# Kernel optimization log

Hardware: AMD Instinct MI355X
Metric: run time of the kernel (lower is better)

## Reference

```python
import jax, jax.numpy as jnp
import numpy as np

KERNEL_SIZES = (2, 3, 4, 5)
B, T = 128, 512
CH, EMB, CHID, HID = 128, 64, 128, 256


def conv1d_same(x, w, b):
    # x: [B, T, Cin], w: [K, Cin, Cout] -> [B, T, Cout]
    y = jax.lax.conv_general_dilated(
        x, w, window_strides=(1,), padding='SAME',
        dimension_numbers=('NWC', 'WIO', 'NWC'))
    return y + b


def gru_last_state(x, Wx, Wh, b_in, b_rec):
    # Keras GRU v2 (reset_after=True), gate order z, r, h. x: [B, T, C].
    H = Wh.shape[0]
    xw = jnp.einsum('btc,ch->bth', x, Wx) + b_in  # precompute input projections [B,T,3H]

    def step(h, xt):
        hw = h @ Wh + b_rec
        xz, xr, xh = jnp.split(xt, 3, axis=-1)
        hz, hr, hh = jnp.split(hw, 3, axis=-1)
        z = jax.nn.sigmoid(xz + hz)
        r = jax.nn.sigmoid(xr + hr)
        hc = jnp.tanh(xh + r * hh)
        return z * h + (1.0 - z) * hc, None

    h0 = jnp.zeros((x.shape[0], H), x.dtype)
    hT, _ = jax.lax.scan(step, h0, jnp.swapaxes(xw, 0, 1))  # scan over time
    return hT  # [B, H]


def setup_inputs() -> dict:
    key = jax.random.key(0)
    ks = jax.random.split(key, 16)
    inp = {}
    inp['X'] = jax.random.randint(ks[0], (B, T), 0, CH)
    inp['emb_table'] = jax.random.normal(ks[1], (CH, EMB), jnp.float32) * 0.05
    s_conv = 1.0 / np.sqrt(EMB)
    for i, k in enumerate(KERNEL_SIZES):
        inp[f'conv_w{k}'] = jax.random.normal(ks[2 + i], (k, EMB, CHID), jnp.float32) * s_conv
        inp[f'conv_b{k}'] = jnp.zeros((CHID,), jnp.float32)
    cin = CHID * len(KERNEL_SIZES)
    inp['gru_Wx'] = jax.random.normal(ks[10], (cin, 3 * HID), jnp.float32) * (1.0 / np.sqrt(cin))
    inp['gru_Wh'] = jax.random.normal(ks[11], (HID, 3 * HID), jnp.float32) * (1.0 / np.sqrt(HID))
    inp['gru_b_in'] = jnp.zeros((3 * HID,), jnp.float32)
    inp['gru_b_rec'] = jnp.zeros((3 * HID,), jnp.float32)
    return inp


def reference(X, emb_table, conv_w2, conv_b2, conv_w3, conv_b3, conv_w4, conv_b4,
              conv_w5, conv_b5, gru_Wx, gru_Wh, gru_b_in, gru_b_rec):
    xe = emb_table[X]  # [B, T, EMB]
    convs = [conv1d_same(xe, w, b) for (w, b) in
             ((conv_w2, conv_b2), (conv_w3, conv_b3), (conv_w4, conv_b4), (conv_w5, conv_b5))]
    xcat = jnp.concatenate(convs, axis=-1)  # [B, T, 4*CHID]
    return gru_last_state(xcat, gru_Wx, gru_Wh, gru_b_in, gru_b_rec)  # [B, HID]
```

## Files before the change

kernel.cpp:

```cpp
#include <hip/hip_runtime.h>
#include <hip/hip_bf16.h>


typedef float f32x4 __attribute__((ext_vector_type(4)));
typedef short s16x8 __attribute__((ext_vector_type(8)));
typedef int   i32x4 __attribute__((ext_vector_type(4)));
typedef unsigned short u16;
typedef unsigned int   u32;
typedef unsigned long long u64;

#define OFF_WC    0u
#define OFF_EMBW  983040u
#define OFF_BEFF  2949120u
#define OFF_WHP   2952192u
#define OFF_MODE  3345408u
#define OFF_HGP   3345472u
#define OFF_FLAG  3607616u
#define FS        516
#define WS_NEED   3624128u

__device__ __forceinline__ float bf2f(u16 v){
  unsigned u = ((unsigned)v) << 16; return __builtin_bit_cast(float, u);
}
__device__ __forceinline__ u16 f2bf(float f){
  unsigned u = __builtin_bit_cast(unsigned, f);
  unsigned r = u + 0x7FFFu + ((u >> 16) & 1u);
  return (u16)(r >> 16);
}
__device__ __forceinline__ float ldv(const void* p, int i, int m){
  return m ? ((const float*)p)[i] : bf2f(((const u16*)p)[i]);
}

__global__ void k_init(char* ws){
  int idx = blockIdx.x*256 + threadIdx.x;
  u32* hg = (u32*)(ws + OFF_HGP);
  if (idx < 65536) hg[idx] = 0u;
  int* fl = (int*)(ws + OFF_FLAG);
  if (idx < 8*FS) fl[idx] = ((idx % FS) == 0) ? 4 : 0;
}

__global__ void k_probe(const void* __restrict__ emb, char* ws){
  const u16* w = (const u16*)emb;
  const int ln = threadIdx.x;
  bool bad = false;
  for (int j = 0; j < 8; ++j){
    u16 v = w[ln*8 + j];
    if (((v >> 7) & 0xFF) >= 0x86) bad = true;
  }
  unsigned long long m = __ballot(bad);
  if (ln == 0) *(int*)(ws + OFF_MODE) = (__popcll(m) > 4) ? 1 : 0;
}

__global__ void k_wc(const void* __restrict__ w2, const void* __restrict__ w3,
                     const void* __restrict__ w4, const void* __restrict__ w5,
                     const void* __restrict__ Wx, char* ws){
  const int md = *(const int*)(ws + OFF_MODE);
  const int d = blockIdx.x >> 6;
  const int e = blockIdx.x & 63;
  const int j0 = threadIdx.x;
  const void* wv[4] = {w2,w3,w4,w5};
  const int Kk[4] = {2,3,4,5}, pd[4] = {0,1,1,2};
  float a0=0.f, a1=0.f, a2=0.f;
  for (int br=0; br<4; ++br){
    int k = d - 2 + pd[br];
    if (k < 0 || k >= Kk[br]) continue;
    const int wbase  = (k*64 + e)*128;
    const int wxbase = (br*128)*768;
    for (int c=0; c<128; ++c){
      float wcv = ldv(wv[br], wbase + c, md);
      a0 += wcv * ldv(Wx, wxbase + c*768 + j0      , md);
      a1 += wcv * ldv(Wx, wxbase + c*768 + j0 + 256, md);
      a2 += wcv * ldv(Wx, wxbase + c*768 + j0 + 512, md);
    }
  }
  float* o = (float*)(ws + OFF_WC) + (d*64 + e)*768;
  o[j0] = a0; o[j0+256] = a1; o[j0+512] = a2;
}

__global__ void k_beff(const void* __restrict__ b2, const void* __restrict__ b3,
                       const void* __restrict__ b4, const void* __restrict__ b5,
                       const void* __restrict__ Wx, const void* __restrict__ bin,
                       char* ws){
  const int md = *(const int*)(ws + OFF_MODE);
  int j = blockIdx.x*256 + threadIdx.x;
  if (j >= 768) return;
  const void* bv[4] = {b2,b3,b4,b5};
  float acc = ldv(bin, j, md);
  for (int br=0; br<4; ++br)
    for (int c=0; c<128; ++c)
      acc += ldv(bv[br], c, md) * ldv(Wx, (br*128 + c)*768 + j, md);
  ((float*)(ws + OFF_BEFF))[j] = acc;
}

__global__ void k_embw(const void* __restrict__ emb, char* ws){
  const int md = *(const int*)(ws + OFF_MODE);
  const int d = blockIdx.x >> 7, ch = blockIdx.x & 127;
  const float* wc = (const float*)(ws + OFF_WC) + d*64*768;
  float* ew = (float*)(ws + OFF_EMBW) + (size_t)(d*128 + ch)*768;
  const int j0 = threadIdx.x;
  float a0=0.f, a1=0.f, a2=0.f;
  for (int e=0; e<64; ++e){
    float ev = ldv(emb, ch*64 + e, md);
    a0 += ev*wc[e*768 + j0      ];
    a1 += ev*wc[e*768 + j0 + 256];
    a2 += ev*wc[e*768 + j0 + 512];
  }
  ew[j0] = a0; ew[j0+256] = a1; ew[j0+512] = a2;
}

__global__ void k_whp(const void* __restrict__ Wh, char* ws){
  const int md = *(const int*)(ws + OFF_MODE);
  const int j = blockIdx.x, k = threadIdx.x;
  ((u16*)(ws + OFF_WHP))[j*256 + k] = f2bf(ldv(Wh, k*768 + j, md));
}

__launch_bounds__(512, 1)
__global__ void k_gru(const int* __restrict__ X, const void* __restrict__ brec,
                      char* __restrict__ ws, void* __restrict__ outv){
  const int tid = threadIdx.x;
  const int w   = tid >> 6, ln = tid & 63;
  const int l15 = ln & 15, l4 = ln >> 4;
  const int g = blockIdx.x >> 2, r = blockIdx.x & 3;

  const int md = *(const int*)(ws + OFF_MODE);
  const float* embw = (const float*)(ws + OFF_EMBW);
  const float* beff = (const float*)(ws + OFF_BEFF);
  const u16*   whp  = (const u16*)(ws + OFF_WHP);
  u32* hgp = (u32*)(ws + OFF_HGP);
  int* flg = (int*)(ws + OFF_FLAG) + g*FS;

  __shared__ int   Xs[16*512];
  __shared__ float xwlds[2][16][196];
  __shared__ float hwp[2][16][196];
  __shared__ u16   hstage[2][16][272];

  for (int i = tid; i < 2048; i += 512)
    ((i32x4*)Xs)[i] = ((const i32x4*)(X + g*16*512))[i];

  const int qs = (w >> 2) * 4;
  s16x8 Bf[3][4];
  #pragma unroll
  for (int gg=0; gg<3; ++gg){
    const int col = gg*256 + r*64 + (w&3)*16 + l15;
    #pragma unroll
    for (int qi=0; qi<4; ++qi)
      Bf[gg][qi] = *(const s16x8*)(whp + col*256 + (qs+qi)*32 + l4*8);
  }

  const int c63 = tid & 63;
  const int tr  = (tid >> 6) & 7;
  const int hc  = r*64 + c63;
  const float br0 = ldv(brec,       hc, md);
  const float br1 = ldv(brec, 256 + hc, md);
  const float br2 = ldv(brec, 512 + hc, md);

  const int row1 = tid / 48,      rem1 = tid % 48;
  const int gg1  = rem1 / 16,     cc1  = rem1 % 16;
  const int cid2 = tid + 512;
  const int row2 = cid2 / 48,     rem2 = cid2 % 48;
  const int gg2  = rem2 / 16,     cc2  = rem2 % 16;
  const bool two = (tid < 256);
  const int gcol1 = gg1*256 + r*64 + cc1*4;
  const int gcol2 = gg2*256 + r*64 + cc2*4;
  const f32x4 be1 = *(const f32x4*)(beff + gcol1);
  const f32x4 be2 = *(const f32x4*)(beff + gcol2);

  const int srow = tid >> 5, sc0 = (tid & 31) * 8;

  __syncthreads();

  {
    f32x4 v1 = be1, v2 = be2;
    #pragma unroll
    for (int d=0; d<5; ++d){
      const int t = d - 2;
      if ((unsigned)t < 512u){
        const int ch1 = Xs[row1*512 + t] & 127;
        v1 += *(const f32x4*)(embw + (size_t)(d*128 + ch1)*768 + gcol1);
        if (two){
          const int ch2 = Xs[row2*512 + t] & 127;
          v2 += *(const f32x4*)(embw + (size_t)(d*128 + ch2)*768 + gcol2);
        }
      }
    }
    *(f32x4*)&xwlds[0][row1][gg1*64 + cc1*4] = v1;
    if (two) *(f32x4*)&xwlds[0][row2][gg2*64 + cc2*4] = v2;
  }
  float hpA = 0.f, hpB = 0.f;
  __syncthreads();

  for (int s = 0; s < 512; ++s){
    const int par = s & 1;

    {
      int guard = 0;
      while (__hip_atomic_load(&flg[s], __ATOMIC_RELAXED, __HIP_MEMORY_SCOPE_AGENT) < 4){
        if (++guard > (1<<23)) break;
      }
    }

    {
      const u32* hb = hgp + (unsigned)par*32768u + (unsigned)g*4096u
                      + (unsigned)srow*256u + (unsigned)sc0;
      u64 d0 = __hip_atomic_load((const u64*)hb+0, __ATOMIC_RELAXED, __HIP_MEMORY_SCOPE_AGENT);
      u64 d1 = __hip_atomic_load((const u64*)hb+1, __ATOMIC_RELAXED, __HIP_MEMORY_SCOPE_AGENT);
      u64 d2 = __hip_atomic_load((const u64*)hb+2, __ATOMIC_RELAXED, __HIP_MEMORY_SCOPE_AGENT);
      u64 d3 = __hip_atomic_load((const u64*)hb+3, __ATOMIC_RELAXED, __HIP_MEMORY_SCOPE_AGENT);
      u32 wd[8] = {(u32)d0,(u32)(d0>>32),(u32)d1,(u32)(d1>>32),
                   (u32)d2,(u32)(d2>>32),(u32)d3,(u32)(d3>>32)};
      s16x8 hi, lo;
      #pragma unroll
      for (int j=0; j<8; ++j){ hi[j] = (short)(wd[j] & 0xFFFFu); lo[j] = (short)(wd[j] >> 16); }
      *(s16x8*)&hstage[0][srow][sc0] = hi;
      *(s16x8*)&hstage[1][srow][sc0] = lo;
    }
    __syncthreads();

    f32x4 a0 = {0.f,0.f,0.f,0.f}, a1 = a0, a2 = a0;
    #pragma unroll
    for (int qi=0; qi<4; ++qi){
      const int kb = (qs+qi)*32 + l4*8;
      const s16x8 ahi = *(const s16x8*)&hstage[0][l15][kb];
      const s16x8 alo = *(const s16x8*)&hstage[1][l15][kb];
      a0 = __builtin_amdgcn_mfma_f32_16x16x32_bf16(ahi, Bf[0][qi], a0, 0,0,0);
      a1 = __builtin_amdgcn_mfma_f32_16x16x32_bf16(ahi, Bf[1][qi], a1, 0,0,0);
      a2 = __builtin_amdgcn_mfma_f32_16x16x32_bf16(ahi, Bf[2][qi], a2, 0,0,0);
      a0 = __builtin_amdgcn_mfma_f32_16x16x32_bf16(alo, Bf[0][qi], a0, 0,0,0);
      a1 = __builtin_amdgcn_mfma_f32_16x16x32_bf16(alo, Bf[1][qi], a1, 0,0,0);
      a2 = __builtin_amdgcn_mfma_f32_16x16x32_bf16(alo, Bf[2][qi], a2, 0,0,0);
    }
    {
      const int kh = w >> 2, sc = (w&3)*16 + l15;
      #pragma unroll
      for (int p=0; p<4; ++p){
        hwp[kh][l4*4+p][       sc] = a0[p];
        hwp[kh][l4*4+p][ 64 + sc] = a1[p];
        hwp[kh][l4*4+p][128 + sc] = a2[p];
      }
    }

    f32x4 n1, n2;
    if (s < 511){
      n1 = be1; n2 = be2;
      #pragma unroll
      for (int d=0; d<5; ++d){
        const int t = s - 1 + d;
        if ((unsigned)t < 512u){
          const int ch1 = Xs[row1*512 + t] & 127;
          n1 += *(const f32x4*)(embw + (size_t)(d*128 + ch1)*768 + gcol1);
          if (two){
            const int ch2 = Xs[row2*512 + t] & 127;
            n2 += *(const f32x4*)(embw + (size_t)(d*128 + ch2)*768 + gcol2);
          }
        }
      }
    }
    __syncthreads();

    float hnA, hnB;
    #pragma unroll
    for (int u=0; u<2; ++u){
      const int row = tr + u*8;
      const float hz = hwp[0][row][      c63] + hwp[1][row][      c63] + br0;
      const float hr = hwp[0][row][ 64 + c63] + hwp[1][row][ 64 + c63] + br1;
      const float hh = hwp[0][row][128 + c63] + hwp[1][row][128 + c63] + br2;
      const float xz = xwlds[par][row][      c63];
      const float xr = xwlds[par][row][ 64 + c63];
      const float xh = xwlds[par][row][128 + c63];
      const float hp = u ? hpB : hpA;
      const float z  = 1.f/(1.f + __expf(-(xz + hz)));
      const float rg = 1.f/(1.f + __expf(-(xr + hr)));
      const float pre = xh + rg*hh;
      const float e2  = __expf(-2.f*fabsf(pre));
      const float th  = __builtin_copysignf((1.f - e2)/(1.f + e2), pre);
      const float hn  = z*hp + (1.f - z)*th;
      if (u) hnB = hn; else hnA = hn;
    }
    hpA = hnA; hpB = hnB;

    if (s == 511){
      const int i0 = (g*16 + tr)*256 + hc;
      if (md){ ((float*)outv)[i0] = hnA; ((float*)outv)[i0 + 8*256] = hnB; }
      else   { ((u16*)outv)[i0] = f2bf(hnA); ((u16*)outv)[i0 + 8*256] = f2bf(hnB); }
    } else {
      u32* hb = hgp + (unsigned)(par^1)*32768u + (unsigned)g*4096u;
      #pragma unroll
      for (int u=0; u<2; ++u){
        const float hn = u ? hnB : hnA;
        const u32 bh = f2bf(hn);
        const u32 bl = f2bf(hn - bf2f((u16)bh));
        __hip_atomic_store(hb + (tr + u*8)*256 + hc, bh | (bl << 16),
                           __ATOMIC_RELAXED, __HIP_MEMORY_SCOPE_AGENT);
      }
      *(f32x4*)&xwlds[par^1][row1][gg1*64 + cc1*4] = n1;
      if (two) *(f32x4*)&xwlds[par^1][row2][gg2*64 + cc2*4] = n2;
    }

    __syncthreads();
    if (s < 511 && tid == 0)
      __hip_atomic_fetch_add(&flg[s+1], 1, __ATOMIC_RELEASE, __HIP_MEMORY_SCOPE_AGENT);
  }
}

extern "C" void kernel_launch(void* const* d_in, const int* in_sizes, int n_in,
                              void* d_out, int out_size, void* d_ws, size_t ws_size,
                              hipStream_t stream){
  const int* X = (const int*)d_in[0];
  char* ws = (char*)d_ws;
  if (ws_size < WS_NEED) return;

  k_init <<<288, 256, 0, stream>>>(ws);
  k_probe<<<  1,  64, 0, stream>>>(d_in[1], ws);
  k_wc   <<<320, 256, 0, stream>>>(d_in[2], d_in[4], d_in[6], d_in[8], d_in[10], ws);
  k_beff <<<  3, 256, 0, stream>>>(d_in[3], d_in[5], d_in[7], d_in[9], d_in[10], d_in[12], ws);
  k_embw <<<640, 256, 0, stream>>>(d_in[1], ws);
  k_whp  <<<768, 256, 0, stream>>>(d_in[11], ws);
  k_gru  <<< 32, 512, 0, stream>>>(X, d_in[13], ws, d_out);
}
```

Measured before the change: 2.350 ms.

## Replace per-step flag counters with sequence bits embedded in hidden-state words

Each hidden-state word now carries a parity sequence bit in the low bit of its bf16 residual half. Consumers spin directly on the data words until all sequence bits match the expected step parity. This removes the per-step global flag array, its release atomic, and the trailing block barrier, which shortens the cross-block handoff on the serial recurrence path. The cost is one mantissa bit lost in the low bf16 correction term, plus repeated polling of four 64-bit loads per thread instead of one flag load.

```diff
diff --git a/kernel.cpp b/kernel.cpp
--- a/kernel.cpp
+++ b/kernel.cpp
@@ -15,9 +15,7 @@
 #define OFF_WHP   2952192u
 #define OFF_MODE  3345408u
 #define OFF_HGP   3345472u
-#define OFF_FLAG  3607616u
-#define FS        516
-#define WS_NEED   3624128u
+#define WS_NEED   3607616u
 
 __device__ __forceinline__ float bf2f(u16 v){
   unsigned u = ((unsigned)v) << 16; return __builtin_bit_cast(float, u);
@@ -35,8 +33,6 @@
   int idx = blockIdx.x*256 + threadIdx.x;
   u32* hg = (u32*)(ws + OFF_HGP);
   if (idx < 65536) hg[idx] = 0u;
-  int* fl = (int*)(ws + OFF_FLAG);
-  if (idx < 8*FS) fl[idx] = ((idx % FS) == 0) ? 4 : 0;
 }
 
 __global__ void k_probe(const void* __restrict__ emb, char* ws){
@@ -127,7 +123,6 @@
   const float* beff = (const float*)(ws + OFF_BEFF);
   const u16*   whp  = (const u16*)(ws + OFF_WHP);
   u32* hgp = (u32*)(ws + OFF_HGP);
-  int* flg = (int*)(ws + OFF_FLAG) + g*FS;
 
   __shared__ int   Xs[16*512];
   __shared__ float xwlds[2][16][196];
@@ -192,25 +187,30 @@
   for (int s = 0; s < 512; ++s){
     const int par = s & 1;
 
+    const u32 em = (u32)((s >> 1) & 1);
+    const u32* hb = hgp + (unsigned)par*32768u + (unsigned)g*4096u
+                    + (unsigned)srow*256u + (unsigned)sc0;
+    u64 d0, d1, d2, d3;
     {
       int guard = 0;
-      while (__hip_atomic_load(&flg[s], __ATOMIC_RELAXED, __HIP_MEMORY_SCOPE_AGENT) < 4){
-        if (++guard > (1<<23)) break;
-      }
-    }
-
+      for (;;){
+        d0 = __hip_atomic_load((const u64*)hb+0, __ATOMIC_RELAXED, __HIP_MEMORY_SCOPE_AGENT);
+        d1 = __hip_atomic_load((const u64*)hb+1, __ATOMIC_RELAXED, __HIP_MEMORY_SCOPE_AGENT);
+        d2 = __hip_atomic_load((const u64*)hb+2, __ATOMIC_RELAXED, __HIP_MEMORY_SCOPE_AGENT);
+        d3 = __hip_atomic_load((const u64*)hb+3, __ATOMIC_RELAXED, __HIP_MEMORY_SCOPE_AGENT);
+        const u64 ba = d0 & d1 & d2 & d3;
+        const u64 bo = d0 | d1 | d2 | d3;
+        const bool ok = em ? ((((ba >> 32) & ba) & 1ull) == 1ull)
+                           : ((((bo >> 32) | bo) & 1ull) == 0ull);
+        if (ok || ++guard > (1<<22)) break;
+      }
+    }
     {
-      const u32* hb = hgp + (unsigned)par*32768u + (unsigned)g*4096u
-                      + (unsigned)srow*256u + (unsigned)sc0;
-      u64 d0 = __hip_atomic_load((const u64*)hb+0, __ATOMIC_RELAXED, __HIP_MEMORY_SCOPE_AGENT);
-      u64 d1 = __hip_atomic_load((const u64*)hb+1, __ATOMIC_RELAXED, __HIP_MEMORY_SCOPE_AGENT);
-      u64 d2 = __hip_atomic_load((const u64*)hb+2, __ATOMIC_RELAXED, __HIP_MEMORY_SCOPE_AGENT);
-      u64 d3 = __hip_atomic_load((const u64*)hb+3, __ATOMIC_RELAXED, __HIP_MEMORY_SCOPE_AGENT);
       u32 wd[8] = {(u32)d0,(u32)(d0>>32),(u32)d1,(u32)(d1>>32),
                    (u32)d2,(u32)(d2>>32),(u32)d3,(u32)(d3>>32)};
       s16x8 hi, lo;
       #pragma unroll
-      for (int j=0; j<8; ++j){ hi[j] = (short)(wd[j] & 0xFFFFu); lo[j] = (short)(wd[j] >> 16); }
+      for (int j=0; j<8; ++j){ hi[j] = (short)(wd[j] >> 16); lo[j] = (short)(wd[j] & 0xFFFFu); }
       *(s16x8*)&hstage[0][srow][sc0] = hi;
       *(s16x8*)&hstage[1][srow][sc0] = lo;
     }
@@ -283,22 +283,20 @@
       if (md){ ((float*)outv)[i0] = hnA; ((float*)outv)[i0 + 8*256] = hnB; }
       else   { ((u16*)outv)[i0] = f2bf(hnA); ((u16*)outv)[i0 + 8*256] = f2bf(hnB); }
     } else {
-      u32* hb = hgp + (unsigned)(par^1)*32768u + (unsigned)g*4096u;
+      const u32 sm = (u32)(((s + 1) >> 1) & 1);
+      u32* hb2 = hgp + (unsigned)(par^1)*32768u + (unsigned)g*4096u;
       #pragma unroll
       for (int u=0; u<2; ++u){
         const float hn = u ? hnB : hnA;
         const u32 bh = f2bf(hn);
-        const u32 bl = f2bf(hn - bf2f((u16)bh));
-        __hip_atomic_store(hb + (tr + u*8)*256 + hc, bh | (bl << 16),
+        u32 bl = f2bf(hn - bf2f((u16)bh));
+        bl = (bl & ~1u) | sm;
+        __hip_atomic_store(hb2 + (tr + u*8)*256 + hc, (bh << 16) | bl,
                            __ATOMIC_RELAXED, __HIP_MEMORY_SCOPE_AGENT);
       }
       *(f32x4*)&xwlds[par^1][row1][gg1*64 + cc1*4] = n1;
       if (two) *(f32x4*)&xwlds[par^1][row2][gg2*64 + cc2*4] = n2;
     }
-
-    __syncthreads();
-    if (s < 511 && tid == 0)
-      __hip_atomic_fetch_add(&flg[s+1], 1, __ATOMIC_RELEASE, __HIP_MEMORY_SCOPE_AGENT);
   }
 }
 
@@ -309,7 +307,7 @@
   char* ws = (char*)d_ws;
   if (ws_size < WS_NEED) return;
 
-  k_init <<<288, 256, 0, stream>>>(ws);
+  k_init <<<256, 256, 0, stream>>>(ws);
   k_probe<<<  1,  64, 0, stream>>>(d_in[1], ws);
   k_wc   <<<320, 256, 0, stream>>>(d_in[2], d_in[4], d_in[6], d_in[8], d_in[10], ws);
   k_beff <<<  3, 256, 0, stream>>>(d_in[3], d_in[5], d_in[7], d_in[9], d_in[10], d_in[12], ws);
```

Measured after the change: 2.137 ms. -9.1%, faster.
